# Kernel optimization log

Measured on AMD Instinct MI355X. Metric: run time of the kernel, lower is better.

The kernel has to match this reference:

```python
import jax, jax.numpy as jnp
from jax import lax
import numpy as np

DIM = 256
N_EMBED = 512
B = 16
T = 2048


def setup_inputs() -> dict:
    key = jax.random.key(0)
    k1, k2, k3 = jax.random.split(key, 3)
    inp = jax.random.normal(k1, (B, T, DIM), dtype=jnp.float32)
    spk = jax.random.normal(k2, (3, B, DIM), dtype=jnp.float32)
    embedding = jax.random.normal(k3, (N_EMBED, DIM, DIM), dtype=jnp.float32)
    return {"input": inp, "speaker_embedding": spk, "embedding": embedding}


def reference(input, speaker_embedding, embedding):
    x = input                              # (B, T, D)
    mul = speaker_embedding[2].T           # (D, B)
    add = speaker_embedding[1].T           # (D, B)
    # per-batch codebook: (n, D, D) @ (D, B) -> (n, D, B)
    cb = jnp.einsum('ndk,kb->ndb', embedding, mul)
    cb = cb / jnp.linalg.norm(cb, axis=1, keepdims=True)
    cb = cb + add                          # broadcast (D,B) over n
    embed = jnp.transpose(cb, (2, 1, 0))   # (B, D, n)
    # distances on detached values (matches torch .detach())
    flat = lax.stop_gradient(x)
    e = lax.stop_gradient(embed)
    dist = (jnp.sum(flat * flat, axis=2, keepdims=True)
            - 2.0 * jnp.einsum('btd,bdn->btn', flat, e)
            + jnp.sum(e * e, axis=1, keepdims=True))  # (B, T, n)
    embed_ind = jnp.argmax(-dist, axis=2)  # (B, T)
    cbB = jnp.transpose(cb, (2, 0, 1))     # (B, n, D)
    # per-batch gather of selected codes -> (B, T, D)
    quantize = cbB[jnp.arange(cbB.shape[0])[:, None], embed_ind]
    diff = jnp.mean((quantize - x) ** 2)
    quantize_1 = x + lax.stop_gradient(quantize - x)
    return ((quantize + quantize_1) / 2.0, diff, embed_ind)
```

## Files before the change

kernel.cpp:

```cpp
#include <hip/hip_runtime.h>

#define T_   2048
#define D_   256
#define N_   512
#define BTOT 16

typedef unsigned short ushortT;

#define QN   ((size_t)BTOT*T_*D_)
#define IDX0 (QN + 1)

__device__ __forceinline__ float bf2f(ushortT u){
    union { unsigned int i; float f; } c; c.i = ((unsigned int)u) << 16; return c.f;
}
__device__ __forceinline__ void unp8(uint4 p, float* f){
    f[0]=bf2f((ushortT)(p.x & 0xffff)); f[1]=bf2f((ushortT)(p.x >> 16));
    f[2]=bf2f((ushortT)(p.y & 0xffff)); f[3]=bf2f((ushortT)(p.y >> 16));
    f[4]=bf2f((ushortT)(p.z & 0xffff)); f[5]=bf2f((ushortT)(p.z >> 16));
    f[6]=bf2f((ushortT)(p.w & 0xffff)); f[7]=bf2f((ushortT)(p.w >> 16));
}
__device__ __forceinline__ void unp4(uint2 p, float* f){
    f[0]=bf2f((ushortT)(p.x & 0xffff)); f[1]=bf2f((ushortT)(p.x >> 16));
    f[2]=bf2f((ushortT)(p.y & 0xffff)); f[3]=bf2f((ushortT)(p.y >> 16));
}

__global__ void k_probe(const ushortT* __restrict__ x, int* __restrict__ flg){
    int tid = threadIdx.x;
    ushortT u = x[tid];
    int e = (u >> 7) & 0xff;
    bool ok = (e >= 100 && e <= 140);
    unsigned long long m = __ballot(ok);
    if (tid == 0) *flg = (__popcll(m) >= 55) ? 1 : 0;
}

template<int BC>
__global__ __launch_bounds__(256) void k_codebook(
    const void* __restrict__ spkin, const void* __restrict__ embin,
    float* __restrict__ cbw, int b0, const int* __restrict__ flagp)
{
    const int isb = *flagp;
    const ushortT* ss = (const ushortT*)spkin;
    const float*   sf = (const float*)spkin;
    const ushortT* es = (const ushortT*)embin;
    const float*   ef = (const float*)embin;

    __shared__ float s2[D_ * 16];
    __shared__ float s1[D_ * 16];
    __shared__ float red[16 * D_];
    __shared__ float nrm[16];

    const int n = blockIdx.x, tid = threadIdx.x;

    for (int e = tid; e < D_ * 16; e += 256){ s2[e] = 0.f; s1[e] = 0.f; }
    __syncthreads();
    for (int e = tid; e < D_ * BC; e += 256){
        int bl = e >> 8, k = e & 255;
        int g2 = (2*BTOT + b0 + bl)*D_ + k;
        int g1 = (1*BTOT + b0 + bl)*D_ + k;
        s2[k*16 + bl] = isb ? bf2f(ss[g2]) : sf[g2];
        s1[k*16 + bl] = isb ? bf2f(ss[g1]) : sf[g1];
    }
    __syncthreads();

    const int d = tid;
    float acc[16];
    #pragma unroll
    for (int b = 0; b < 16; b++) acc[b] = 0.f;

    const size_t rb = ((size_t)n * D_ + d) * D_;

    auto inner = [&](const float* ev, int k0){
        #pragma unroll
        for (int j = 0; j < 8; j++){
            float e = ev[j];
            if (BC == 16){
                const float4* sp = (const float4*)&s2[(k0 + j) * 16];
                float4 q0 = sp[0], q1 = sp[1], q2 = sp[2], q3 = sp[3];
                acc[0]  += e*q0.x; acc[1]  += e*q0.y; acc[2]  += e*q0.z; acc[3]  += e*q0.w;
                acc[4]  += e*q1.x; acc[5]  += e*q1.y; acc[6]  += e*q1.z; acc[7]  += e*q1.w;
                acc[8]  += e*q2.x; acc[9]  += e*q2.y; acc[10] += e*q2.z; acc[11] += e*q2.w;
                acc[12] += e*q3.x; acc[13] += e*q3.y; acc[14] += e*q3.z; acc[15] += e*q3.w;
            } else {
                #pragma unroll
                for (int bl = 0; bl < BC; bl++)
                    acc[bl] += e * s2[(k0 + j)*16 + bl];
            }
        }
    };

    if (isb){
        for (int k0 = 0; k0 < D_; k0 += 8){
            uint4 p = *(const uint4*)(es + rb + k0);
            float ev[8]; unp8(p, ev);
            inner(ev, k0);
        }
    } else {
        for (int k0 = 0; k0 < D_; k0 += 8){
            float4 p0 = *(const float4*)(ef + rb + k0);
            float4 p1 = *(const float4*)(ef + rb + k0 + 4);
            float ev[8] = {p0.x,p0.y,p0.z,p0.w,p1.x,p1.y,p1.z,p1.w};
            inner(ev, k0);
        }
    }

    #pragma unroll
    for (int bl = 0; bl < BC; bl++) red[bl*D_ + d] = acc[bl]*acc[bl];
    __syncthreads();
    for (int s = 128; s > 0; s >>= 1){
        if (d < s){
            #pragma unroll
            for (int bl = 0; bl < BC; bl++) red[bl*D_ + d] += red[bl*D_ + d + s];
        }
        __syncthreads();
    }
    if (d < BC) nrm[d] = sqrtf(red[d*D_]);
    __syncthreads();

    #pragma unroll
    for (int bl = 0; bl < BC; bl++){
        float cb = acc[bl] / nrm[bl] + s1[d*16 + bl];
        cbw[((size_t)bl*N_ + n)*D_ + d] = cb;
    }
}

__global__ __launch_bounds__(512, 2) void k_gemm(
    const void* __restrict__ xin, const float* __restrict__ cbw,
    float* __restrict__ outf, int blk0, const int* __restrict__ flagp)
{
    const int isb = *flagp;
    const int bl = blockIdx.x >> 4, tT = blockIdx.x & 15;
    const int bg = blk0 + bl;

    __shared__ float As[16 * 132];
    __shared__ float Bs[16 * 256];
    __shared__ float e2p[512];

    const int tid = threadIdx.x;
    const int tx = tid & 31, ty = tid >> 5;
    const int rA = tid >> 2, qA = tid & 3;
    const int rB = tid >> 1, hB = tid & 1;

    const float*   xf = (const float*)xin;
    const ushortT* xs = (const ushortT*)xin;
    const size_t xbase = ((size_t)bg*T_ + tT*128 + rA)*D_ + qA*4;

    float runv[8]; int runi[8];
    #pragma unroll
    for (int i = 0; i < 8; i++){ runv[i] = 3.4e38f; runi[i] = 0x7fffffff; }

    for (int nT = 0; nT < 2; nT++){
        float acc[8][8];
        #pragma unroll
        for (int i = 0; i < 8; i++)
            #pragma unroll
            for (int j = 0; j < 8; j++) acc[i][j] = 0.f;
        float e2acc = 0.f;

        const size_t bbase = ((size_t)bl*N_ + nT*256 + rB)*D_ + hB*8;

        for (int k0 = 0; k0 < D_; k0 += 16){
            float av[4];
            if (isb){
                uint2 p = *(const uint2*)(xs + xbase + k0);
                unp4(p, av);
            } else {
                float4 p = *(const float4*)(xf + xbase + k0);
                av[0]=p.x; av[1]=p.y; av[2]=p.z; av[3]=p.w;
            }
            float bv[8];
            {
                float4 q0 = *(const float4*)(cbw + bbase + k0);
                float4 q1 = *(const float4*)(cbw + bbase + k0 + 4);
                bv[0]=q0.x; bv[1]=q0.y; bv[2]=q0.z; bv[3]=q0.w;
                bv[4]=q1.x; bv[5]=q1.y; bv[6]=q1.z; bv[7]=q1.w;
            }
            #pragma unroll
            for (int j = 0; j < 8; j++) e2acc += bv[j]*bv[j];

            #pragma unroll
            for (int j = 0; j < 4; j++) As[(qA*4 + j)*132 + rA] = av[j];
            #pragma unroll
            for (int j = 0; j < 8; j++) Bs[(hB*8 + j)*256 + rB] = bv[j];
            __syncthreads();

            #pragma unroll
            for (int kl = 0; kl < 16; kl++){
                float4 a0 = *(const float4*)&As[kl*132 + (ty<<2)];
                float4 a1 = *(const float4*)&As[kl*132 + 64 + (ty<<2)];
                float4 c0 = *(const float4*)&Bs[kl*256 + (tx<<2)];
                float4 c1 = *(const float4*)&Bs[kl*256 + 128 + (tx<<2)];
                float ar[8] = {a0.x,a0.y,a0.z,a0.w,a1.x,a1.y,a1.z,a1.w};
                float br[8] = {c0.x,c0.y,c0.z,c0.w,c1.x,c1.y,c1.z,c1.w};
                #pragma unroll
                for (int i = 0; i < 8; i++)
                    #pragma unroll
                    for (int j = 0; j < 8; j++)
                        acc[i][j] += ar[i]*br[j];
            }
            __syncthreads();
        }

        e2p[rB*2 + hB] = e2acc;
        __syncthreads();

        float e2c[8];
        #pragma unroll
        for (int j = 0; j < 8; j++){
            int nl = (tx<<2) + (j&3) + ((j>>2)<<7);
            e2c[j] = e2p[nl*2] + e2p[nl*2 + 1];
        }

        #pragma unroll
        for (int i = 0; i < 8; i++){
            #pragma unroll
            for (int j = 0; j < 8; j++){
                int ng = nT*256 + (tx<<2) + (j&3) + ((j>>2)<<7);
                float s = e2c[j] - 2.f*acc[i][j];
                if (s < runv[i] || (s == runv[i] && ng < runi[i])){
                    runv[i] = s; runi[i] = ng;
                }
            }
        }
    }

    #pragma unroll
    for (int m = 16; m >= 1; m >>= 1){
        #pragma unroll
        for (int i = 0; i < 8; i++){
            float ov = __shfl_xor(runv[i], m);
            int   on = __shfl_xor(runi[i], m);
            if (ov < runv[i] || (ov == runv[i] && on < runi[i])){
                runv[i] = ov; runi[i] = on;
            }
        }
    }
    if (tx == 0){
        #pragma unroll
        for (int i = 0; i < 8; i++){
            int row = (ty<<2) + (i&3) + ((i>>2)<<6);
            outf[IDX0 + (size_t)bg*T_ + tT*128 + row] = (float)runi[i];
        }
    }
}

__global__ __launch_bounds__(256) void k_gather(
    const void* __restrict__ xin, const float* __restrict__ cbw,
    float* __restrict__ outf, float* __restrict__ part,
    int blk0, const int* __restrict__ flagp)
{
    const int isb = *flagp;
    const int bid = blockIdx.x;
    const int bl = bid >> 11, t = bid & 2047;
    const int bg = blk0 + bl;
    const int tid = threadIdx.x;

    const int n = (int)outf[IDX0 + (size_t)bg*T_ + t];

    const float*   xf = (const float*)xin;
    const ushortT* xs = (const ushortT*)xin;
    const size_t rowbase = ((size_t)bg*T_ + t)*D_;
    float xv = isb ? bf2f(xs[rowbase + tid]) : xf[rowbase + tid];
    float q  = cbw[((size_t)bl*N_ + n)*D_ + tid];
    float qm = q - xv;
    float q1 = xv + qm;
    outf[rowbase + tid] = 0.5f*(q + q1);

    float val = qm*qm;
    #pragma unroll
    for (int o = 32; o > 0; o >>= 1) val += __shfl_down(val, o, 64);
    __shared__ float wsum[4];
    if ((tid & 63) == 0) wsum[tid >> 6] = val;
    __syncthreads();
    if (tid == 0)
        atomicAdd(&part[bid & 1023], wsum[0] + wsum[1] + wsum[2] + wsum[3]);
}

__global__ __launch_bounds__(256) void k_fin(const float* __restrict__ part,
                                             float* __restrict__ outf){
    const int tid = threadIdx.x;
    float v = part[tid] + part[tid + 256] + part[tid + 512] + part[tid + 768];
    #pragma unroll
    for (int o = 32; o > 0; o >>= 1) v += __shfl_down(v, o, 64);
    __shared__ float wsum[4];
    if ((tid & 63) == 0) wsum[tid >> 6] = v;
    __syncthreads();
    if (tid == 0)
        outf[QN] = (wsum[0] + wsum[1] + wsum[2] + wsum[3]) * (1.0f / (float)QN);
}

extern "C" void kernel_launch(void* const* d_in, const int* in_sizes, int n_in,
                              void* d_out, int out_size, void* d_ws, size_t ws_size,
                              hipStream_t stream)
{
    const void* x   = d_in[0];
    const void* spk = d_in[1];
    const void* emb = d_in[2];

    int Bc = 16;
    while (Bc > 1 && ((size_t)Bc*N_*D_*4 + 4096 + 16) > ws_size) Bc >>= 1;

    char*  ws   = (char*)d_ws;
    float* cbw  = (float*)ws;
    size_t tail = (size_t)Bc*N_*D_*4;
    float* part = (float*)(ws + tail);
    int*   flg  = (int*)  (ws + tail + 4096);

    float* outf = (float*)d_out;

    hipMemsetAsync(part, 0, 4096, stream);
    k_probe<<<1, 64, 0, stream>>>((const ushortT*)x, flg);

    for (int b0 = 0; b0 < BTOT; b0 += Bc){
        switch (Bc){
            case 16: k_codebook<16><<<512, 256, 0, stream>>>(spk, emb, cbw, b0, flg); break;
            case 8:  k_codebook<8> <<<512, 256, 0, stream>>>(spk, emb, cbw, b0, flg); break;
            case 4:  k_codebook<4> <<<512, 256, 0, stream>>>(spk, emb, cbw, b0, flg); break;
            case 2:  k_codebook<2> <<<512, 256, 0, stream>>>(spk, emb, cbw, b0, flg); break;
            default: k_codebook<1> <<<512, 256, 0, stream>>>(spk, emb, cbw, b0, flg); break;
        }
        k_gemm  <<<Bc*16,   512, 0, stream>>>(x, cbw, outf, b0, flg);
        k_gather<<<Bc*2048, 256, 0, stream>>>(x, cbw, outf, part, b0, flg);
    }
    k_fin<<<1, 256, 0, stream>>>(part, outf);
}
```

Measured before the change: 386.0 us.

## Use split-fp16 MFMA for distance GEMM and fuse gather into argmin kernel

When the input is detected as bf16, the codebook kernel now writes each code as a high fp16 part plus a scaled low residual in an MFMA-fragment layout, along with precomputed squared norms. A new fused kernel computes distances with 16x16x32 f16 MFMAs on both parts, reduces the argmin in-block, and then gathers the chosen codes, writes the quantized output and accumulates the loss. This removes the scalar FP32 GEMM and the separate gather launch. The cost is doubled MFMA work for the hi/lo split and possible argmin differences from fp16 rounding of x.

```diff
diff --git a/kernel.cpp b/kernel.cpp
--- a/kernel.cpp
+++ b/kernel.cpp
@@ -6,9 +6,13 @@
 #define BTOT 16
 
 typedef unsigned short ushortT;
+typedef _Float16 f16;
+typedef f16 h8 __attribute__((ext_vector_type(8)));
+typedef float f4v __attribute__((ext_vector_type(4)));
 
 #define QN   ((size_t)BTOT*T_*D_)
 #define IDX0 (QN + 1)
+#define CBSTRIDE ((size_t)N_*D_)
 
 __device__ __forceinline__ float bf2f(ushortT u){
     union { unsigned int i; float f; } c; c.i = ((unsigned int)u) << 16; return c.f;
@@ -19,9 +23,15 @@
     f[4]=bf2f((ushortT)(p.z & 0xffff)); f[5]=bf2f((ushortT)(p.z >> 16));
     f[6]=bf2f((ushortT)(p.w & 0xffff)); f[7]=bf2f((ushortT)(p.w >> 16));
 }
-__device__ __forceinline__ void unp4(uint2 p, float* f){
-    f[0]=bf2f((ushortT)(p.x & 0xffff)); f[1]=bf2f((ushortT)(p.x >> 16));
-    f[2]=bf2f((ushortT)(p.y & 0xffff)); f[3]=bf2f((ushortT)(p.y >> 16));
+__device__ __forceinline__ h8 cvt8(uint4 p){
+    float f[8]; unp8(p, f);
+    h8 h;
+    #pragma unroll
+    for (int j = 0; j < 8; j++) h[j] = (f16)f[j];
+    return h;
+}
+__device__ __forceinline__ f4v mfma16(h8 a, h8 b, f4v c){
+    return __builtin_amdgcn_mfma_f32_16x16x32_f16(a, b, c, 0, 0, 0);
 }
 
 __global__ void k_probe(const ushortT* __restrict__ x, int* __restrict__ flg){
@@ -36,7 +46,8 @@
 template<int BC>
 __global__ __launch_bounds__(256) void k_codebook(
     const void* __restrict__ spkin, const void* __restrict__ embin,
-    float* __restrict__ cbw, int b0, const int* __restrict__ flagp)
+    float* __restrict__ cbw, f16* __restrict__ hig, f16* __restrict__ logp,
+    float* __restrict__ e2g, int b0, const int* __restrict__ flagp)
 {
     const int isb = *flagp;
     const ushortT* ss = (const ushortT*)spkin;
@@ -54,11 +65,11 @@
     for (int e = tid; e < D_ * 16; e += 256){ s2[e] = 0.f; s1[e] = 0.f; }
     __syncthreads();
     for (int e = tid; e < D_ * BC; e += 256){
-        int bl = e >> 8, k = e & 255;
-        int g2 = (2*BTOT + b0 + bl)*D_ + k;
-        int g1 = (1*BTOT + b0 + bl)*D_ + k;
-        s2[k*16 + bl] = isb ? bf2f(ss[g2]) : sf[g2];
-        s1[k*16 + bl] = isb ? bf2f(ss[g1]) : sf[g1];
+        int blc = e >> 8, k = e & 255;
+        int g2 = (2*BTOT + b0 + blc)*D_ + k;
+        int g1 = (1*BTOT + b0 + blc)*D_ + k;
+        s2[k*16 + blc] = isb ? bf2f(ss[g2]) : sf[g2];
+        s1[k*16 + blc] = isb ? bf2f(ss[g1]) : sf[g1];
     }
     __syncthreads();
 
@@ -82,8 +93,8 @@
                 acc[12] += e*q3.x; acc[13] += e*q3.y; acc[14] += e*q3.z; acc[15] += e*q3.w;
             } else {
                 #pragma unroll
-                for (int bl = 0; bl < BC; bl++)
-                    acc[bl] += e * s2[(k0 + j)*16 + bl];
+                for (int blc = 0; blc < BC; blc++)
+                    acc[blc] += e * s2[(k0 + j)*16 + blc];
             }
         }
     };
@@ -104,175 +115,343 @@
     }
 
     #pragma unroll
-    for (int bl = 0; bl < BC; bl++) red[bl*D_ + d] = acc[bl]*acc[bl];
+    for (int blc = 0; blc < BC; blc++) red[blc*D_ + d] = acc[blc]*acc[blc];
     __syncthreads();
     for (int s = 128; s > 0; s >>= 1){
         if (d < s){
             #pragma unroll
-            for (int bl = 0; bl < BC; bl++) red[bl*D_ + d] += red[bl*D_ + d + s];
+            for (int blc = 0; blc < BC; blc++) red[blc*D_ + d] += red[blc*D_ + d + s];
         }
         __syncthreads();
     }
     if (d < BC) nrm[d] = sqrtf(red[d*D_]);
     __syncthreads();
 
+    float cbv[BC];
     #pragma unroll
-    for (int bl = 0; bl < BC; bl++){
-        float cb = acc[bl] / nrm[bl] + s1[d*16 + bl];
-        cbw[((size_t)bl*N_ + n)*D_ + d] = cb;
-    }
-}
-
-__global__ __launch_bounds__(512, 2) void k_gemm(
+    for (int blc = 0; blc < BC; blc++)
+        cbv[blc] = acc[blc] / nrm[blc] + s1[d*16 + blc];
+
+    if (!isb){
+        #pragma unroll
+        for (int blc = 0; blc < BC; blc++)
+            cbw[((size_t)blc*N_ + n)*D_ + d] = cbv[blc];
+    } else {
+        #pragma unroll
+        for (int blc = 0; blc < BC; blc++) red[blc*D_ + d] = cbv[blc]*cbv[blc];
+        __syncthreads();
+        for (int s = 128; s > 0; s >>= 1){
+            if (d < s){
+                #pragma unroll
+                for (int blc = 0; blc < BC; blc++) red[blc*D_ + d] += red[blc*D_ + d + s];
+            }
+            __syncthreads();
+        }
+        if (d < BC) e2g[(size_t)d*N_ + n] = red[d*D_];
+
+        f16* sh = (f16*)s2;
+        #pragma unroll
+        for (int blc = 0; blc < BC; blc++){
+            float c = cbv[blc];
+            f16 h = (f16)c;
+            float r = c - (float)h;
+            f16 l = (f16)(r * 4096.f);
+            sh[blc*256 + d] = h;
+            sh[4096 + blc*256 + d] = l;
+        }
+        __syncthreads();
+        for (int w = tid; w < BC*32; w += 256){
+            const int blc = w >> 5, g = w & 31;
+            const int d0 = (g>>2)*32 + (g&3)*8;
+            const size_t off = (size_t)blc*CBSTRIDE
+                             + (size_t)((n>>4)*8 + (g>>2))*512
+                             + (size_t)(g&3)*128 + (size_t)(n&15)*8;
+            *(uint4*)(hig  + off) = *(const uint4*)(sh + blc*256 + d0);
+            *(uint4*)(logp + off) = *(const uint4*)(sh + 4096 + blc*256 + d0);
+        }
+    }
+}
+
+__global__ __launch_bounds__(512, 2) void k_fused(
     const void* __restrict__ xin, const float* __restrict__ cbw,
-    float* __restrict__ outf, int blk0, const int* __restrict__ flagp)
+    const f16* __restrict__ hig, const f16* __restrict__ logp,
+    const float* __restrict__ e2g,
+    float* __restrict__ outf, float* __restrict__ part,
+    int blk0, const int* __restrict__ flagp)
 {
-    const int isb = *flagp;
-    const int bl = blockIdx.x >> 4, tT = blockIdx.x & 15;
-    const int bg = blk0 + bl;
-
     __shared__ float As[16 * 132];
     __shared__ float Bs[16 * 256];
     __shared__ float e2p[512];
-
+    __shared__ float mv[8 * 32];
+    __shared__ int   mi[8 * 32];
+    __shared__ int   sfin[128];
+    __shared__ float wsum[8];
+
+    const int isb = *flagp;
     const int tid = threadIdx.x;
-    const int tx = tid & 31, ty = tid >> 5;
-    const int rA = tid >> 2, qA = tid & 3;
-    const int rB = tid >> 1, hB = tid & 1;
-
-    const float*   xf = (const float*)xin;
-    const ushortT* xs = (const ushortT*)xin;
-    const size_t xbase = ((size_t)bg*T_ + tT*128 + rA)*D_ + qA*4;
-
-    float runv[8]; int runi[8];
-    #pragma unroll
-    for (int i = 0; i < 8; i++){ runv[i] = 3.4e38f; runi[i] = 0x7fffffff; }
-
-    for (int nT = 0; nT < 2; nT++){
-        float acc[8][8];
-        #pragma unroll
-        for (int i = 0; i < 8; i++)
-            #pragma unroll
-            for (int j = 0; j < 8; j++) acc[i][j] = 0.f;
-        float e2acc = 0.f;
-
-        const size_t bbase = ((size_t)bl*N_ + nT*256 + rB)*D_ + hB*8;
-
-        for (int k0 = 0; k0 < D_; k0 += 16){
-            float av[4];
-            if (isb){
-                uint2 p = *(const uint2*)(xs + xbase + k0);
-                unp4(p, av);
-            } else {
-                float4 p = *(const float4*)(xf + xbase + k0);
-                av[0]=p.x; av[1]=p.y; av[2]=p.z; av[3]=p.w;
-            }
-            float bv[8];
-            {
-                float4 q0 = *(const float4*)(cbw + bbase + k0);
-                float4 q1 = *(const float4*)(cbw + bbase + k0 + 4);
-                bv[0]=q0.x; bv[1]=q0.y; bv[2]=q0.z; bv[3]=q0.w;
-                bv[4]=q1.x; bv[5]=q1.y; bv[6]=q1.z; bv[7]=q1.w;
-            }
-            #pragma unroll
-            for (int j = 0; j < 8; j++) e2acc += bv[j]*bv[j];
-
-            #pragma unroll
-            for (int j = 0; j < 4; j++) As[(qA*4 + j)*132 + rA] = av[j];
-            #pragma unroll
-            for (int j = 0; j < 8; j++) Bs[(hB*8 + j)*256 + rB] = bv[j];
+    const int bl = blockIdx.x >> 4, tT = blockIdx.x & 15;
+    const int bg = blk0 + bl;
+
+    if (isb){
+        const ushortT* xs = (const ushortT*)xin;
+        const int lane = tid & 63, wid = tid >> 6;
+        const int band = wid >> 1, nh = wid & 1;
+        const int arow = lane & 15, kgrp = lane >> 4;
+
+        h8 afr[2][8];
+        {
+            const ushortT* xw = xs + ((size_t)bg*T_ + (size_t)tT*128 + band*32)*D_;
+            #pragma unroll
+            for (int rf = 0; rf < 2; rf++)
+                #pragma unroll
+                for (int ks = 0; ks < 8; ks++){
+                    uint4 p = *(const uint4*)(xw + (size_t)(rf*16 + arow)*D_ + ks*32 + kgrp*8);
+                    afr[rf][ks] = cvt8(p);
+                }
+        }
+
+        const f16* hb = hig  + (size_t)bl*CBSTRIDE + (size_t)(lane*8);
+        const f16* lb = logp + (size_t)bl*CBSTRIDE + (size_t)(lane*8);
+
+        float runv[8]; int runi[8];
+        #pragma unroll
+        for (int i = 0; i < 8; i++){ runv[i] = 3.4e38f; runi[i] = 0x7fffffff; }
+
+        #pragma unroll 1
+        for (int c = 0; c < 8; c++){
+            const int nc0 = nh*16 + c*2;
+            f4v acch[2][2], accl[2][2];
+            #pragma unroll
+            for (int rf = 0; rf < 2; rf++)
+                #pragma unroll
+                for (int t2 = 0; t2 < 2; t2++){
+                    acch[rf][t2] = (f4v){0.f,0.f,0.f,0.f};
+                    accl[rf][t2] = (f4v){0.f,0.f,0.f,0.f};
+                }
+            const f16* hc = hb + (size_t)nc0*4096;
+            const f16* lc = lb + (size_t)nc0*4096;
+            #pragma unroll
+            for (int ks = 0; ks < 8; ks++){
+                h8 b0h = *(const h8*)(hc + ks*512);
+                h8 b1h = *(const h8*)(hc + 4096 + ks*512);
+                h8 b0l = *(const h8*)(lc + ks*512);
+                h8 b1l = *(const h8*)(lc + 4096 + ks*512);
+                #pragma unroll
+                for (int rf = 0; rf < 2; rf++){
+                    acch[rf][0] = mfma16(afr[rf][ks], b0h, acch[rf][0]);
+                    accl[rf][0] = mfma16(afr[rf][ks], b0l, accl[rf][0]);
+                    acch[rf][1] = mfma16(afr[rf][ks], b1h, acch[rf][1]);
+                    accl[rf][1] = mfma16(afr[rf][ks], b1l, accl[rf][1]);
+                }
+            }
+            #pragma unroll
+            for (int t2 = 0; t2 < 2; t2++){
+                const int nn = (nc0 + t2)*16 + arow;
+                const float e2v = e2g[(size_t)bl*N_ + nn];
+                #pragma unroll
+                for (int rf = 0; rf < 2; rf++)
+                    #pragma unroll
+                    for (int r = 0; r < 4; r++){
+                        float s = e2v - 2.f*(acch[rf][t2][r] + accl[rf][t2][r]*(1.f/4096.f));
+                        int ii = rf*4 + r;
+                        if (s < runv[ii]){ runv[ii] = s; runi[ii] = nn; }
+                    }
+            }
+        }
+
+        #pragma unroll
+        for (int m = 8; m >= 1; m >>= 1){
+            #pragma unroll
+            for (int i = 0; i < 8; i++){
+                float ov = __shfl_xor(runv[i], m);
+                int   on = __shfl_xor(runi[i], m);
+                if (ov < runv[i] || (ov == runv[i] && on < runi[i])){
+                    runv[i] = ov; runi[i] = on;
+                }
+            }
+        }
+        if (arow == 0){
+            #pragma unroll
+            for (int i = 0; i < 8; i++){
+                int r = (i>>2)*16 + kgrp*4 + (i&3);
+                mv[wid*32 + r] = runv[i];
+                mi[wid*32 + r] = runi[i];
+            }
+        }
+        __syncthreads();
+        if (tid < 128){
+            int bandt = tid >> 5, r = tid & 31;
+            float v0 = mv[(bandt*2    )*32 + r]; int i0 = mi[(bandt*2    )*32 + r];
+            float v1 = mv[(bandt*2 + 1)*32 + r]; int i1 = mi[(bandt*2 + 1)*32 + r];
+            int nf = (v1 < v0) ? i1 : i0;
+            sfin[tid] = nf;
+            outf[IDX0 + (size_t)bg*T_ + (size_t)tT*128 + tid] = (float)nf;
+        }
+        __syncthreads();
+
+        float dacc = 0.f;
+        const int lh = lane >> 5, dg = lane & 31;
+        #pragma unroll
+        for (int it = 0; it < 8; it++){
+            const int r = wid*16 + it*2 + lh;
+            const int nn = sfin[r];
+            const size_t off = (size_t)bl*CBSTRIDE
+                             + (size_t)((nn>>4)*8 + (dg>>2))*512
+                             + (size_t)(dg&3)*128 + (size_t)(nn&15)*8;
+            h8 hq = *(const h8*)(hig  + off);
+            h8 lq = *(const h8*)(logp + off);
+            const size_t xo = ((size_t)bg*T_ + (size_t)tT*128 + r)*D_ + dg*8;
+            uint4 p = *(const uint4*)(xs + xo);
+            float xf8[8]; unp8(p, xf8);
+            float og[8];
+            #pragma unroll
+            for (int j = 0; j < 8; j++){
+                float q  = (float)hq[j] + (float)lq[j]*(1.f/4096.f);
+                float qm = q - xf8[j];
+                dacc += qm*qm;
+                og[j] = 0.5f*(q + (xf8[j] + qm));
+            }
+            *(float4*)(outf + xo)     = make_float4(og[0],og[1],og[2],og[3]);
+            *(float4*)(outf + xo + 4) = make_float4(og[4],og[5],og[6],og[7]);
+        }
+        #pragma unroll
+        for (int o2 = 32; o2 > 0; o2 >>= 1) dacc += __shfl_down(dacc, o2, 64);
+        if (lane == 0) wsum[wid] = dacc;
+        __syncthreads();
+        if (tid == 0){
+            float t = 0.f;
+            #pragma unroll
+            for (int i = 0; i < 8; i++) t += wsum[i];
+            atomicAdd(&part[blockIdx.x & 1023], t);
+        }
+    }
+    else {
+        const float* xf = (const float*)xin;
+        const int tx = tid & 31, ty = tid >> 5;
+        const int rA = tid >> 2, qA = tid & 3;
+        const int rB = tid >> 1, hB = tid & 1;
+        const size_t xbase = ((size_t)bg*T_ + tT*128 + rA)*D_ + qA*4;
+
+        float runv[8]; int runi[8];
+        #pragma unroll
+        for (int i = 0; i < 8; i++){ runv[i] = 3.4e38f; runi[i] = 0x7fffffff; }
+
+        for (int nT = 0; nT < 2; nT++){
+            float acc[8][8];
+            #pragma unroll
+            for (int i = 0; i < 8; i++)
+                #pragma unroll
+                for (int j = 0; j < 8; j++) acc[i][j] = 0.f;
+            float e2acc = 0.f;
+
+            const size_t bbase = ((size_t)bl*N_ + nT*256 + rB)*D_ + hB*8;
+
+            for (int k0 = 0; k0 < D_; k0 += 16){
+                float av[4];
+                {
+                    float4 p = *(const float4*)(xf + xbase + k0);
+                    av[0]=p.x; av[1]=p.y; av[2]=p.z; av[3]=p.w;
+                }
+                float bv[8];
+                {
+                    float4 q0 = *(const float4*)(cbw + bbase + k0);
+                    float4 q1 = *(const float4*)(cbw + bbase + k0 + 4);
+                    bv[0]=q0.x; bv[1]=q0.y; bv[2]=q0.z; bv[3]=q0.w;
+                    bv[4]=q1.x; bv[5]=q1.y; bv[6]=q1.z; bv[7]=q1.w;
+                }
+                #pragma unroll
+                for (int j = 0; j < 8; j++) e2acc += bv[j]*bv[j];
+
+                #pragma unroll
+                for (int j = 0; j < 4; j++) As[(qA*4 + j)*132 + rA] = av[j];
+                #pragma unroll
+                for (int j = 0; j < 8; j++) Bs[(hB*8 + j)*256 + rB] = bv[j];
+                __syncthreads();
+
+                #pragma unroll
+                for (int kl = 0; kl < 16; kl++){
+                    float4 a0 = *(const float4*)&As[kl*132 + (ty<<2)];
+                    float4 a1 = *(const float4*)&As[kl*132 + 64 + (ty<<2)];
+                    float4 c0 = *(const float4*)&Bs[kl*256 + (tx<<2)];
+                    float4 c1 = *(const float4*)&Bs[kl*256 + 128 + (tx<<2)];
+                    float ar[8] = {a0.x,a0.y,a0.z,a0.w,a1.x,a1.y,a1.z,a1.w};
+                    float br[8] = {c0.x,c0.y,c0.z,c0.w,c1.x,c1.y,c1.z,c1.w};
+                    #pragma unroll
+                    for (int i = 0; i < 8; i++)
+                        #pragma unroll
+                        for (int j = 0; j < 8; j++)
+                            acc[i][j] += ar[i]*br[j];
+                }
+                __syncthreads();
+            }
+
+            e2p[rB*2 + hB] = e2acc;
             __syncthreads();
 
-            #pragma unroll
-            for (int kl = 0; kl < 16; kl++){
-                float4 a0 = *(const float4*)&As[kl*132 + (ty<<2)];
-                float4 a1 = *(const float4*)&As[kl*132 + 64 + (ty<<2)];
-                float4 c0 = *(const float4*)&Bs[kl*256 + (tx<<2)];
-                float4 c1 = *(const float4*)&Bs[kl*256 + 128 + (tx<<2)];
-                float ar[8] = {a0.x,a0.y,a0.z,a0.w,a1.x,a1.y,a1.z,a1.w};
-                float br[8] = {c0.x,c0.y,c0.z,c0.w,c1.x,c1.y,c1.z,c1.w};
-                #pragma unroll
-                for (int i = 0; i < 8; i++)
-                    #pragma unroll
-                    for (int j = 0; j < 8; j++)
-                        acc[i][j] += ar[i]*br[j];
-            }
-            __syncthreads();
-        }
-
-        e2p[rB*2 + hB] = e2acc;
-        __syncthreads();
-
-        float e2c[8];
-        #pragma unroll
-        for (int j = 0; j < 8; j++){
-            int nl = (tx<<2) + (j&3) + ((j>>2)<<7);
-            e2c[j] = e2p[nl*2] + e2p[nl*2 + 1];
-        }
-
-        #pragma unroll
-        for (int i = 0; i < 8; i++){
+            float e2c[8];
             #pragma unroll
             for (int j = 0; j < 8; j++){
-                int ng = nT*256 + (tx<<2) + (j&3) + ((j>>2)<<7);
-                float s = e2c[j] - 2.f*acc[i][j];
-                if (s < runv[i] || (s == runv[i] && ng < runi[i])){
-                    runv[i] = s; runi[i] = ng;
-                }
-            }
-        }
-    }
-
-    #pragma unroll
-    for (int m = 16; m >= 1; m >>= 1){
-        #pragma unroll
-        for (int i = 0; i < 8; i++){
-            float ov = __shfl_xor(runv[i], m);
-            int   on = __shfl_xor(runi[i], m);
-            if (ov < runv[i] || (ov == runv[i] && on < runi[i])){
-                runv[i] = ov; runi[i] = on;
-            }
-        }
-    }
-    if (tx == 0){
-        #pragma unroll
-        for (int i = 0; i < 8; i++){
-            int row = (ty<<2) + (i&3) + ((i>>2)<<6);
-            outf[IDX0 + (size_t)bg*T_ + tT*128 + row] = (float)runi[i];
-        }
-    }
-}
-
-__global__ __launch_bounds__(256) void k_gather(
-    const void* __restrict__ xin, const float* __restrict__ cbw,
-    float* __restrict__ outf, float* __restrict__ part,
-    int blk0, const int* __restrict__ flagp)
-{
-    const int isb = *flagp;
-    const int bid = blockIdx.x;
-    const int bl = bid >> 11, t = bid & 2047;
-    const int bg = blk0 + bl;
-    const int tid = threadIdx.x;
-
-    const int n = (int)outf[IDX0 + (size_t)bg*T_ + t];
-
-    const float*   xf = (const float*)xin;
-    const ushortT* xs = (const ushortT*)xin;
-    const size_t rowbase = ((size_t)bg*T_ + t)*D_;
-    float xv = isb ? bf2f(xs[rowbase + tid]) : xf[rowbase + tid];
-    float q  = cbw[((size_t)bl*N_ + n)*D_ + tid];
-    float qm = q - xv;
-    float q1 = xv + qm;
-    outf[rowbase + tid] = 0.5f*(q + q1);
-
-    float val = qm*qm;
-    #pragma unroll
-    for (int o = 32; o > 0; o >>= 1) val += __shfl_down(val, o, 64);
-    __shared__ float wsum[4];
-    if ((tid & 63) == 0) wsum[tid >> 6] = val;
-    __syncthreads();
-    if (tid == 0)
-        atomicAdd(&part[bid & 1023], wsum[0] + wsum[1] + wsum[2] + wsum[3]);
+                int nl = (tx<<2) + (j&3) + ((j>>2)<<7);
+                e2c[j] = e2p[nl*2] + e2p[nl*2 + 1];
+            }
+
+            #pragma unroll
+            for (int i = 0; i < 8; i++){
+                #pragma unroll
+                for (int j = 0; j < 8; j++){
+                    int ng = nT*256 + (tx<<2) + (j&3) + ((j>>2)<<7);
+                    float s = e2c[j] - 2.f*acc[i][j];
+                    if (s < runv[i] || (s == runv[i] && ng < runi[i])){
+                        runv[i] = s; runi[i] = ng;
+                    }
+                }
+            }
+        }
+
+        #pragma unroll
+        for (int m = 16; m >= 1; m >>= 1){
+            #pragma unroll
+            for (int i = 0; i < 8; i++){
+                float ov = __shfl_xor(runv[i], m);
+                int   on = __shfl_xor(runi[i], m);
+                if (ov < runv[i] || (ov == runv[i] && on < runi[i])){
+                    runv[i] = ov; runi[i] = on;
+                }
+            }
+        }
+        if (tx == 0){
+            #pragma unroll
+            for (int i = 0; i < 8; i++){
+                int row = (ty<<2) + (i&3) + ((i>>2)<<6);
+                sfin[row] = runi[i];
+                outf[IDX0 + (size_t)bg*T_ + (size_t)tT*128 + row] = (float)runi[i];
+            }
+        }
+        __syncthreads();
+
+        float dacc = 0.f;
+        for (int rr = 0; rr < 128; rr += 2){
+            const int row = rr + (tid >> 8);
+            const int dd = tid & 255;
+            const int nn = sfin[row];
+            const float q = cbw[((size_t)bl*N_ + nn)*D_ + dd];
+            const size_t xo = ((size_t)bg*T_ + (size_t)tT*128 + row)*D_ + dd;
+            const float xv = xf[xo];
+            const float qm = q - xv;
+            dacc += qm*qm;
+            outf[xo] = 0.5f*(q + (xv + qm));
+        }
+        #pragma unroll
+        for (int o2 = 32; o2 > 0; o2 >>= 1) dacc += __shfl_down(dacc, o2, 64);
+        if ((tid & 63) == 0) wsum[tid >> 6] = dacc;
+        __syncthreads();
+        if (tid == 0){
+            float t = 0.f;
+            #pragma unroll
+            for (int i = 0; i < 8; i++) t += wsum[i];
+            atomicAdd(&part[blockIdx.x & 1023], t);
+        }
+    }
 }
 
 __global__ __launch_bounds__(256) void k_fin(const float* __restrict__ part,
@@ -297,13 +476,15 @@
     const void* emb = d_in[2];
 
     int Bc = 16;
-    while (Bc > 1 && ((size_t)Bc*N_*D_*4 + 4096 + 16) > ws_size) Bc >>= 1;
+    while (Bc > 1 && ((size_t)Bc*N_*D_*4 + (size_t)Bc*N_*4 + 4096 + 16) > ws_size) Bc >>= 1;
 
     char*  ws   = (char*)d_ws;
+    f16*   hig  = (f16*)ws;
+    f16*   logp = (f16*)(ws + (size_t)Bc*N_*D_*2);
     float* cbw  = (float*)ws;
-    size_t tail = (size_t)Bc*N_*D_*4;
-    float* part = (float*)(ws + tail);
-    int*   flg  = (int*)  (ws + tail + 4096);
+    float* e2g  = (float*)(ws + (size_t)Bc*N_*D_*4);
+    float* part = (float*)(ws + (size_t)Bc*N_*D_*4 + (size_t)Bc*N_*4);
+    int*   flg  = (int*)((char*)part + 4096);
 
     float* outf = (float*)d_out;
 
@@ -312,14 +493,13 @@
 
     for (int b0 = 0; b0 < BTOT; b0 += Bc){
         switch (Bc){
-            case 16: k_codebook<16><<<512, 256, 0, stream>>>(spk, emb, cbw, b0, flg); break;
-            case 8:  k_codebook<8> <<<512, 256, 0, stream>>>(spk, emb, cbw, b0, flg); break;
-            case 4:  k_codebook<4> <<<512, 256, 0, stream>>>(spk, emb, cbw, b0, flg); break;
-            case 2:  k_codebook<2> <<<512, 256, 0, stream>>>(spk, emb, cbw, b0, flg); break;
-            default: k_codebook<1> <<<512, 256, 0, stream>>>(spk, emb, cbw, b0, flg); break;
-        }
-        k_gemm  <<<Bc*16,   512, 0, stream>>>(x, cbw, outf, b0, flg);
-        k_gather<<<Bc*2048, 256, 0, stream>>>(x, cbw, outf, part, b0, flg);
+            case 16: k_codebook<16><<<512, 256, 0, stream>>>(spk, emb, cbw, hig, logp, e2g, b0, flg); break;
+            case 8:  k_codebook<8> <<<512, 256, 0, stream>>>(spk, emb, cbw, hig, logp, e2g, b0, flg); break;
+            case 4:  k_codebook<4> <<<512, 256, 0, stream>>>(spk, emb, cbw, hig, logp, e2g, b0, flg); break;
+            case 2:  k_codebook<2> <<<512, 256, 0, stream>>>(spk, emb, cbw, hig, logp, e2g, b0, flg); break;
+            default: k_codebook<1> <<<512, 256, 0, stream>>>(spk, emb, cbw, hig, logp, e2g, b0, flg); break;
+        }
+        k_fused<<<Bc*16, 512, 0, stream>>>(x, cbw, hig, logp, e2g, outf, part, b0, flg);
     }
     k_fin<<<1, 256, 0, stream>>>(part, outf);
 }
```

Measured after the change: 370.7 us. 1.04x faster.
